# Performance work log

Measured on AMD Instinct MI355X. Metric: run time of the kernel, lower is better.

The kernel has to match this reference:

```python
import jax, jax.numpy as jnp
import numpy as np

B, T, D, NH, L = 8192, 100, 44, 64, 8  # batch, seq/ode steps, obs_dim, rnn hidden, latent


def setup_inputs() -> dict:
    key = jax.random.key(0)
    ks = jax.random.split(key, 12)
    s = 0.1
    return {
        "x": jax.random.normal(ks[0], (B, T, D), jnp.float32),
        "mask": jax.random.randint(ks[1], (B, T, D), 0, 2).astype(jnp.float32),
        "epsilon": jax.random.normal(ks[2], (B, L), jnp.float32),
        "Wi2h": jax.random.normal(ks[3], (D + NH, NH), jnp.float32) * s,
        "bi2h": jnp.zeros((NH,), jnp.float32),
        "Wh2o": jax.random.normal(ks[4], (NH, 2 * L), jnp.float32) * s,
        "bh2o": jnp.zeros((2 * L,), jnp.float32),
        "Wf1": jax.random.normal(ks[5], (L, NH), jnp.float32) * s,
        "bf1": jnp.zeros((NH,), jnp.float32),
        "Wf2": jax.random.normal(ks[6], (NH, NH), jnp.float32) * s,
        "bf2": jnp.zeros((NH,), jnp.float32),
        "Wf3": jax.random.normal(ks[7], (NH, L), jnp.float32) * s,
        "bf3": jnp.zeros((L,), jnp.float32),
        "Wd1": jax.random.normal(ks[8], (L, NH), jnp.float32) * s,
        "bd1": jnp.zeros((NH,), jnp.float32),
        "Wd2": jax.random.normal(ks[9], (NH, D), jnp.float32) * s,
        "bd2": jnp.zeros((D,), jnp.float32),
    }


def reference(x, mask, epsilon, Wi2h, bi2h, Wh2o, bh2o,
              Wf1, bf1, Wf2, bf2, Wf3, bf3, Wd1, bd1, Wd2, bd2):
    masked_x = x * mask  # [B,T,D]

    # --- reverse-time recognition RNN (scan over time, reversed) ---
    def rnn_step(h, obs):
        h = jnp.tanh(jnp.concatenate([obs, h], axis=1) @ Wi2h + bi2h)
        return h, None

    xs_rev = jnp.transpose(masked_x[:, ::-1, :], (1, 0, 2))  # [T,B,D]
    h0 = jnp.zeros((x.shape[0], Wi2h.shape[1]), x.dtype)
    h_final, _ = jax.lax.scan(rnn_step, h0, xs_rev)
    out = h_final @ Wh2o + bh2o  # [B,2L]
    qz0_mean, qz0_logvar = out[:, :L], out[:, L:]

    # reparameterized latent sample
    z0 = epsilon * jnp.exp(0.5 * qz0_logvar) + qz0_mean  # [B,L]

    # --- latent ODE dynamics, fixed-step RK4 over ts = linspace(0,1,100) ---
    def f(z):
        h1 = jax.nn.elu(z @ Wf1 + bf1)
        h2 = jax.nn.elu(h1 @ Wf2 + bf2)
        return h2 @ Wf3 + bf3

    dt = jnp.asarray(1.0 / (T - 1), x.dtype)

    def rk4_step(z, _):
        k1 = f(z)
        k2 = f(z + 0.5 * dt * k1)
        k3 = f(z + 0.5 * dt * k2)
        k4 = f(z + dt * k3)
        zn = z + (dt / 6.0) * (k1 + 2.0 * k2 + 2.0 * k3 + k4)
        return zn, zn

    _, zs = jax.lax.scan(rk4_step, z0, None, length=T - 1)  # [T-1,B,L]
    pred_z = jnp.transpose(jnp.concatenate([z0[None], zs], axis=0), (1, 0, 2))  # [B,T,L]

    # --- decoder ---
    pred_x = jax.nn.relu(pred_z @ Wd1 + bd1) @ Wd2 + bd2  # [B,T,D]

    # fill observed entries back in
    updated_x = jnp.where(masked_x != 0, masked_x, pred_x)

    # --- loss ---
    noise_logvar = 2.0 * jnp.log(jnp.asarray(0.3, x.dtype))
    log2pi = jnp.log(jnp.asarray(2.0 * np.pi, x.dtype))
    logpx = (-0.5 * (log2pi + noise_logvar +
                     (x - updated_x) ** 2 / jnp.exp(noise_logvar))).sum((-1, -2))  # [B]
    kl = (-0.5 * qz0_logvar + (jnp.exp(qz0_logvar) + qz0_mean ** 2) / 2.0 - 0.5).sum(-1)  # [B]
    loss = jnp.mean(-logpx + kl)
    return loss
```

## Files before the change

kernel.cpp:

```cpp
#include <hip/hip_runtime.h>
#include <stdint.h>


constexpr int B_ = 8192, T_ = 100, D_ = 44, NH_ = 64, L_ = 8;

typedef float f32x4 __attribute__((ext_vector_type(4)));
typedef uint32_t u32x2 __attribute__((ext_vector_type(2)));

#if __has_builtin(__builtin_amdgcn_mfma_f32_16x16x16bf16_1k)
typedef short frag16 __attribute__((ext_vector_type(4)));
#define MFMA16(a, b, c) __builtin_amdgcn_mfma_f32_16x16x16bf16_1k(a, b, c, 0, 0, 0)
#define USE_F16 0
#elif __has_builtin(__builtin_amdgcn_mfma_f32_16x16x16_bf16_1k)
typedef short frag16 __attribute__((ext_vector_type(4)));
#define MFMA16(a, b, c) __builtin_amdgcn_mfma_f32_16x16x16_bf16_1k(a, b, c, 0, 0, 0)
#define USE_F16 0
#elif __has_builtin(__builtin_amdgcn_mfma_f32_16x16x16_bf16)
typedef __bf16 frag16 __attribute__((ext_vector_type(4)));
#define MFMA16(a, b, c) __builtin_amdgcn_mfma_f32_16x16x16_bf16(a, b, c, 0, 0, 0)
#define USE_F16 0
#else
typedef _Float16 frag16 __attribute__((ext_vector_type(4)));
#define MFMA16(a, b, c) __builtin_amdgcn_mfma_f32_16x16x16f16(a, b, c, 0, 0, 0)
#define USE_F16 1
#endif

__device__ __forceinline__ float fexp2(float x) { return __builtin_amdgcn_exp2f(x); }
__device__ __forceinline__ float frcp(float x) { return __builtin_amdgcn_rcpf(x); }
__device__ __forceinline__ float fexp(float x) { return fexp2(x * 1.44269504088896341f); }
__device__ __forceinline__ float tanh_f(float x) {
  float e = fexp2(x * 2.88539008177792681f);
  return 1.0f - 2.0f * frcp(e + 1.0f);
}
__device__ __forceinline__ float elu_f(float x) { return x > 0.0f ? x : (fexp(x) - 1.0f); }

__device__ __forceinline__ uint32_t EW(float v) {
#if USE_F16
  return (uint32_t)__builtin_bit_cast(unsigned short, (_Float16)v);
#else
  return (uint32_t)__builtin_bit_cast(unsigned short, (__bf16)v);
#endif
}
__device__ __forceinline__ uint32_t PK2(float lo, float hi) { return EW(lo) | (EW(hi) << 16); }
__device__ __forceinline__ frag16 fr4(float a, float b, float c, float d) {
  u32x2 u = {PK2(a, b), PK2(c, d)};
  return __builtin_bit_cast(frag16, u);
}
__device__ __forceinline__ frag16 frpk(f32x4 v) {
  u32x2 u = {PK2(v[0], v[1]), PK2(v[2], v[3])};
  return __builtin_bit_cast(frag16, u);
}
__device__ __forceinline__ float f4get(const float4& f, int i) {
  return i == 0 ? f.x : (i == 1 ? f.y : (i == 2 ? f.z : f.w));
}

__global__ __launch_bounds__(128) void fused_kernel(
    const float* __restrict__ x, const float* __restrict__ mask,
    const float* __restrict__ eps,
    const float* __restrict__ Wi2h, const float* __restrict__ bi2h,
    const float* __restrict__ Wh2o, const float* __restrict__ bh2o,
    const float* __restrict__ Wf1, const float* __restrict__ bf1,
    const float* __restrict__ Wf2, const float* __restrict__ bf2,
    const float* __restrict__ Wf3, const float* __restrict__ bf3,
    const float* __restrict__ Wd1, const float* __restrict__ bd1,
    const float* __restrict__ Wd2, const float* __restrict__ bd2,
    float* __restrict__ part) {
  const int tid = threadIdx.x;
  const int wid = tid >> 6;
  const int lane = tid & 63;
  const int c = lane & 15, q = lane >> 4;
  const int r0 = blockIdx.x * 16;
  const f32x4 fzero = {0.f, 0.f, 0.f, 0.f};

  __shared__ __align__(16) uint32_t ring[6400];
  __shared__ __align__(16) float pcring[8192];
  __shared__ uint32_t flags[104];
  __shared__ uint32_t w1prog;
  __shared__ uint32_t w0cons;
  __shared__ float sse_sh;

  if (tid < 104) flags[tid] = 0u;
  if (tid == 0) { w1prog = 0u; w0cons = 0u; }
  __syncthreads();

  float klt = 0.0f;

  if (wid == 0) {
    frag16 Ah[4][4];
#pragma unroll
    for (int tau = 0; tau < 4; ++tau)
#pragma unroll
      for (int kc = 0; kc < 4; ++kc) {
        const int m = 16 * tau + c;
        float wv[4];
#pragma unroll
        for (int i = 0; i < 4; ++i) wv[i] = Wi2h[(44 + 16 * kc + 4 * q + i) * 64 + m];
        Ah[tau][kc] = fr4(wv[0], wv[1], wv[2], wv[3]);
      }
    frag16 Ah2o[4];
#pragma unroll
    for (int kc = 0; kc < 4; ++kc) {
      float wv[4];
#pragma unroll
      for (int i = 0; i < 4; ++i) wv[i] = Wh2o[(16 * kc + 4 * q + i) * 16 + c];
      Ah2o[kc] = fr4(wv[0], wv[1], wv[2], wv[3]);
    }
    f32x4 bo;
#pragma unroll
    for (int r = 0; r < 4; ++r) bo[r] = bh2o[4 * q + r];

    volatile uint32_t* vprod = &w1prog;
    volatile uint32_t* vcons = &w0cons;

    while (*vprod < 1u) __builtin_amdgcn_s_sleep(1);
    asm volatile("" ::: "memory");
    f32x4 pcur[4], pnext[4];
#pragma unroll
    for (int tau = 0; tau < 4; ++tau)
      pcur[tau] = *(const f32x4*)(pcring + tau * 256 + lane * 4);
    if (lane == 0) *vcons = 1u;

    f32x4 hc[4] = {};
#pragma unroll 1
    for (int s = 0; s < T_; ++s) {
      if ((s & 3) == 0) {
        const uint32_t need = (uint32_t)((s + 5 > T_) ? T_ : s + 5);
        while (*vprod < need) __builtin_amdgcn_s_sleep(1);
        asm volatile("" ::: "memory");
      }
      if (s < T_ - 1) {
        const int sl = (s + 1) & 7;
#pragma unroll
        for (int tau = 0; tau < 4; ++tau)
          pnext[tau] = *(const f32x4*)(pcring + sl * 1024 + tau * 256 + lane * 4);
        if (lane == 0) *vcons = (uint32_t)(s + 2);
      }

      frag16 bh[4];
#pragma unroll
      for (int tau = 0; tau < 4; ++tau) bh[tau] = frpk(hc[tau]);
#pragma unroll
      for (int tau = 0; tau < 4; ++tau) {
        f32x4 p0 = MFMA16(Ah[tau][0], bh[0], pcur[tau]);
        f32x4 p1 = MFMA16(Ah[tau][1], bh[1], fzero);
        f32x4 p2 = MFMA16(Ah[tau][2], bh[2], fzero);
        f32x4 p3 = MFMA16(Ah[tau][3], bh[3], fzero);
#pragma unroll
        for (int r = 0; r < 4; ++r)
          hc[tau][r] = tanh_f((p0[r] + p1[r]) + (p2[r] + p3[r]));
      }
#pragma unroll
      for (int tau = 0; tau < 4; ++tau) pcur[tau] = pnext[tau];
    }

    frag16 bhF[4];
#pragma unroll
    for (int tau = 0; tau < 4; ++tau) bhF[tau] = frpk(hc[tau]);
    f32x4 o = bo;
#pragma unroll
    for (int kc = 0; kc < 4; ++kc) o = MFMA16(Ah2o[kc], bhF[kc], o);

    float lv[4];
#pragma unroll
    for (int r = 0; r < 4; ++r)
      lv[r] = __int_as_float(__shfl(__float_as_int(o[r]), lane + 32, 64));

    f32x4 z = {};
    if (q < 2) {
      const float4 ev = *(const float4*)(eps + (size_t)(r0 + c) * 8 + 4 * q);
#pragma unroll
      for (int r = 0; r < 4; ++r) {
        const float m = o[r];
        z[r] = f4get(ev, r) * fexp(0.5f * lv[r]) + m;
        klt += -0.5f * lv[r] + (fexp(lv[r]) + m * m) * 0.5f - 0.5f;
      }
    }
    klt += __shfl_xor(klt, 1);  klt += __shfl_xor(klt, 2);
    klt += __shfl_xor(klt, 4);  klt += __shfl_xor(klt, 8);
    klt += __shfl_xor(klt, 16); klt += __shfl_xor(klt, 32);

    __builtin_amdgcn_sched_barrier(0);

    frag16 A1[4], A2[4][4], A3[4];
#pragma unroll
    for (int tau = 0; tau < 4; ++tau) {
      float w1[4];
#pragma unroll
      for (int i = 0; i < 4; ++i) {
        const int k = 4 * q + i;
        w1[i] = k < 8 ? Wf1[k * 64 + 16 * tau + c] : (k == 8 ? bf1[16 * tau + c] : 0.0f);
      }
      A1[tau] = fr4(w1[0], w1[1], w1[2], w1[3]);
    }
#pragma unroll
    for (int tau = 0; tau < 4; ++tau)
#pragma unroll
      for (int kc = 0; kc < 4; ++kc) {
        float wv[4];
#pragma unroll
        for (int i = 0; i < 4; ++i) wv[i] = Wf2[(16 * kc + 4 * q + i) * 64 + 16 * tau + c];
        A2[tau][kc] = fr4(wv[0], wv[1], wv[2], wv[3]);
      }
#pragma unroll
    for (int kc = 0; kc < 4; ++kc) {
      float wv[4];
#pragma unroll
      for (int i = 0; i < 4; ++i)
        wv[i] = (c < 8) ? Wf3[(16 * kc + 4 * q + i) * 8 + c] : 0.0f;
      A3[kc] = fr4(wv[0], wv[1], wv[2], wv[3]);
    }
    f32x4 b2_[4], b3_;
#pragma unroll
    for (int tau = 0; tau < 4; ++tau)
#pragma unroll
      for (int r = 0; r < 4; ++r) b2_[tau][r] = bf2[16 * tau + 4 * q + r];
#pragma unroll
    for (int r = 0; r < 4; ++r) b3_[r] = (q < 2) ? bf3[4 * q + r] : 0.0f;

    auto build_bz = [&](f32x4 zv) -> frag16 {
      u32x2 u = {PK2(zv[0], zv[1]), PK2(zv[2], zv[3])};
      if (q == 2) { u[0] = EW(1.0f); u[1] = 0u; }
      else if (q == 3) { u[0] = 0u; u[1] = 0u; }
      return __builtin_bit_cast(frag16, u);
    };

    auto feval = [&](frag16 bz) -> f32x4 {
      frag16 bh[4];
#pragma unroll
      for (int tau = 0; tau < 4; ++tau) {
        f32x4 h = MFMA16(A1[tau], bz, fzero);
#pragma unroll
        for (int r = 0; r < 4; ++r) h[r] = elu_f(h[r]);
        bh[tau] = frpk(h);
      }
      frag16 bg[4];
#pragma unroll
      for (int tau = 0; tau < 4; ++tau) {
        f32x4 g0 = MFMA16(A2[tau][0], bh[0], b2_[tau]);
        f32x4 g1 = MFMA16(A2[tau][1], bh[1], fzero);
        f32x4 g2 = MFMA16(A2[tau][2], bh[2], fzero);
        f32x4 g3 = MFMA16(A2[tau][3], bh[3], fzero);
        f32x4 g;
#pragma unroll
        for (int r = 0; r < 4; ++r) g[r] = elu_f((g0[r] + g1[r]) + (g2[r] + g3[r]));
        bg[tau] = frpk(g);
      }
      f32x4 r0_ = MFMA16(A3[0], bg[0], b3_);
      f32x4 r1_ = MFMA16(A3[1], bg[1], fzero);
      f32x4 r2_ = MFMA16(A3[2], bg[2], fzero);
      f32x4 r3_ = MFMA16(A3[3], bg[3], fzero);
      f32x4 rr;
#pragma unroll
      for (int r = 0; r < 4; ++r) rr[r] = (r0_[r] + r1_[r]) + (r2_[r] + r3_[r]);
      return rr;
    };

    const float dt = 1.0f / (float)(T_ - 1);
    const float hdt = 0.5f * dt;

#pragma unroll 1
    for (int t = 0; t < T_; ++t) {
      if (q < 2) {
        u32x2 v = {PK2(z[0], z[1]), PK2(z[2], z[3])};
        *(u32x2*)(ring + (t * 32 + c * 2 + q) * 2) = v;
      }
      asm volatile("" ::: "memory");
      if (lane == 0) ((volatile uint32_t*)flags)[t] = 1u;

      if (t < T_ - 1) {
        f32x4 k1 = feval(build_bz(z));
        f32x4 zt;
#pragma unroll
        for (int r = 0; r < 4; ++r) zt[r] = z[r] + hdt * k1[r];
        f32x4 k2 = feval(build_bz(zt));
#pragma unroll
        for (int r = 0; r < 4; ++r) zt[r] = z[r] + hdt * k2[r];
        f32x4 k3 = feval(build_bz(zt));
#pragma unroll
        for (int r = 0; r < 4; ++r) zt[r] = z[r] + dt * k3[r];
        f32x4 k4 = feval(build_bz(zt));
#pragma unroll
        for (int r = 0; r < 4; ++r)
          z[r] += (dt / 6.0f) * (k1[r] + 2.0f * (k2[r] + k3[r]) + k4[r]);
      }
    }
  } else {
    const frag16 fgbias = fr4(1.0f, 0.f, 0.f, 0.f);

    frag16 Ao[4][3];
#pragma unroll
    for (int tau = 0; tau < 4; ++tau)
#pragma unroll
      for (int kc = 0; kc < 3; ++kc) {
        const int m = 16 * tau + c;
        float wv[4];
#pragma unroll
        for (int i = 0; i < 4; ++i) {
          const int k = 64 + 16 * kc + 4 * q + i;
          float v = 0.0f;
          if (k < 108) v = Wi2h[(k - 64) * 64 + m];
          else if (k == 108) v = bi2h[m];
          wv[i] = v;
        }
        Ao[tau][kc] = fr4(wv[0], wv[1], wv[2], wv[3]);
      }

    const float* xrowbase = x + (size_t)(r0 + c) * T_ * D_;
    const float* mrowbase = mask + (size_t)(r0 + c) * T_ * D_;

    auto load_obs = [&](int t, float4* xv, float4* mv) {
      const float* xp = xrowbase + (size_t)t * D_;
      const float* mp = mrowbase + (size_t)t * D_;
      xv[0] = *(const float4*)(xp + 4 * q);
      mv[0] = *(const float4*)(mp + 4 * q);
      xv[1] = *(const float4*)(xp + 16 + 4 * q);
      mv[1] = *(const float4*)(mp + 16 + 4 * q);
      float4 zz = {0.f, 0.f, 0.f, 0.f};
      xv[2] = zz; mv[2] = zz;
      if (q < 3) {
        xv[2] = *(const float4*)(xp + 32 + 4 * q);
        mv[2] = *(const float4*)(mp + 32 + 4 * q);
      }
    };
    auto make_ob = [&](const float4* cx, const float4* cm, frag16* ob) {
#pragma unroll
      for (int j = 0; j < 2; ++j) {
        u32x2 u = {PK2(cx[j].x * cm[j].x, cx[j].y * cm[j].y),
                   PK2(cx[j].z * cm[j].z, cx[j].w * cm[j].w)};
        ob[j] = __builtin_bit_cast(frag16, u);
      }
      u32x2 u = {PK2(cx[2].x * cm[2].x, cx[2].y * cm[2].y),
                 PK2(cx[2].z * cm[2].z, cx[2].w * cm[2].w)};
      ob[2] = (q < 3) ? __builtin_bit_cast(frag16, u) : fgbias;
    };

    volatile uint32_t* vcons = &w0cons;
    volatile uint32_t* vprod = &w1prog;

    {
      float4 xo[3], mo[3];
      load_obs(T_ - 1, xo, mo);
#pragma unroll 1
      for (int s1 = 0; s1 < T_; ++s1) {
        const int t = T_ - 1 - s1;
        float4 cx[3], cm[3];
#pragma unroll
        for (int j = 0; j < 3; ++j) { cx[j] = xo[j]; cm[j] = mo[j]; }
        if (t > 0) load_obs(t - 1, xo, mo);

        frag16 ob[3];
        make_ob(cx, cm, ob);
        f32x4 pc[4];
#pragma unroll
        for (int tau = 0; tau < 4; ++tau)
          pc[tau] = MFMA16(Ao[tau][2], ob[2],
                           MFMA16(Ao[tau][1], ob[1],
                                  MFMA16(Ao[tau][0], ob[0], fzero)));

        while ((uint32_t)s1 >= *vcons + 8u) __builtin_amdgcn_s_sleep(1);
        asm volatile("" ::: "memory");
        const int sl = s1 & 7;
#pragma unroll
        for (int tau = 0; tau < 4; ++tau)
          *(f32x4*)(pcring + sl * 1024 + tau * 256 + lane * 4) = pc[tau];
        asm volatile("" ::: "memory");
        if (lane == 0) *vprod = (uint32_t)(s1 + 1);
      }
    }

    frag16 Ad1[4], Ad2[3][4];
#pragma unroll
    for (int tau = 0; tau < 4; ++tau) {
      float wd[4];
#pragma unroll
      for (int i = 0; i < 4; ++i) {
        const int k = 4 * q + i;
        wd[i] = k < 8 ? Wd1[k * 64 + 16 * tau + c] : (k == 8 ? bd1[16 * tau + c] : 0.0f);
      }
      Ad1[tau] = fr4(wd[0], wd[1], wd[2], wd[3]);
    }
#pragma unroll
    for (int tau = 0; tau < 3; ++tau)
#pragma unroll
      for (int kc = 0; kc < 4; ++kc) {
        const int m = 16 * tau + c;
        float wv[4];
#pragma unroll
        for (int i = 0; i < 4; ++i)
          wv[i] = (m < 44) ? Wd2[(16 * kc + 4 * q + i) * 44 + m] : 0.0f;
        Ad2[tau][kc] = fr4(wv[0], wv[1], wv[2], wv[3]);
      }
    f32x4 bd2_[3];
#pragma unroll
    for (int tau = 0; tau < 3; ++tau)
#pragma unroll
      for (int r = 0; r < 4; ++r) {
        const int d = 16 * tau + 4 * q + r;
        bd2_[tau][r] = (d < 44) ? bd2[d] : 0.0f;
      }

    float qacc = 0.0f;
    volatile uint32_t* vf = flags;

#pragma unroll 1
    for (int t = 0; t < T_; ++t) {
      float4 xc[3], mc[3];
#pragma unroll
      for (int tau = 0; tau < 3; ++tau) {
        const int d0 = 16 * tau + 4 * q;
        if (d0 < 44) {
          const size_t off = (size_t)(r0 + c) * T_ * D_ + (size_t)t * D_ + d0;
          xc[tau] = *(const float4*)(x + off);
          mc[tau] = *(const float4*)(mask + off);
        } else {
          float4 zz = {0.f, 0.f, 0.f, 0.f};
          xc[tau] = zz; mc[tau] = zz;
        }
      }

      while (vf[t] == 0u) __builtin_amdgcn_s_sleep(1);
      asm volatile("" ::: "memory");

      frag16 bz;
      {
        u32x2 u = {0u, 0u};
        if (q < 2) u = *(const u32x2*)(ring + (t * 32 + c * 2 + q) * 2);
        else if (q == 2) u[0] = EW(1.0f);
        bz = __builtin_bit_cast(frag16, u);
      }

      frag16 bhd[4];
#pragma unroll
      for (int tau = 0; tau < 4; ++tau) {
        f32x4 hd = MFMA16(Ad1[tau], bz, fzero);
#pragma unroll
        for (int r = 0; r < 4; ++r) hd[r] = fmaxf(hd[r], 0.0f);
        bhd[tau] = frpk(hd);
      }
#pragma unroll
      for (int tau = 0; tau < 3; ++tau) {
        f32x4 p0 = MFMA16(Ad2[tau][0], bhd[0], bd2_[tau]);
        f32x4 p1 = MFMA16(Ad2[tau][1], bhd[1], fzero);
        f32x4 p2 = MFMA16(Ad2[tau][2], bhd[2], fzero);
        f32x4 p3 = MFMA16(Ad2[tau][3], bhd[3], fzero);
        if (16 * tau + 4 * q < 44) {
#pragma unroll
          for (int r = 0; r < 4; ++r) {
            const float p = (p0[r] + p1[r]) + (p2[r] + p3[r]);
            const float xa = f4get(xc[tau], r), ma = f4get(mc[tau], r);
            const float mx = xa * ma;
            const float upd = (mx != 0.0f) ? mx : p;
            const float df = xa - upd;
            qacc += df * df;
          }
        }
      }
    }

    float tot = qacc * (0.5f / 0.09f);
    tot += __shfl_xor(tot, 1);  tot += __shfl_xor(tot, 2);
    tot += __shfl_xor(tot, 4);  tot += __shfl_xor(tot, 8);
    tot += __shfl_xor(tot, 16); tot += __shfl_xor(tot, 32);
    if (lane == 0) sse_sh = tot;
  }

  __syncthreads();
  if (tid == 0) part[blockIdx.x] = sse_sh + klt;
}

__global__ __launch_bounds__(512) void reduce_kernel(const float* __restrict__ part,
                                                     float* __restrict__ out) {
  __shared__ float s[8];
  const int tid = threadIdx.x;
  float v = part[tid];
  v += __shfl_xor(v, 1);  v += __shfl_xor(v, 2);
  v += __shfl_xor(v, 4);  v += __shfl_xor(v, 8);
  v += __shfl_xor(v, 16); v += __shfl_xor(v, 32);
  if ((tid & 63) == 0) s[tid >> 6] = v;
  __syncthreads();
  if (tid == 0) {
    float acc = 0.0f;
#pragma unroll
    for (int i = 0; i < 8; ++i) acc += s[i];
    const float c0 = 0.28503427112126353f;
    out[0] = acc * (1.0f / (float)B_) - (float)(T_ * D_) * c0;
  }
}

extern "C" void kernel_launch(void* const* d_in, const int* in_sizes, int n_in,
                              void* d_out, int out_size, void* d_ws, size_t ws_size,
                              hipStream_t stream) {
  const float* x    = (const float*)d_in[0];
  const float* mask = (const float*)d_in[1];
  const float* eps  = (const float*)d_in[2];
  const float* Wi2h = (const float*)d_in[3];
  const float* bi2h = (const float*)d_in[4];
  const float* Wh2o = (const float*)d_in[5];
  const float* bh2o = (const float*)d_in[6];
  const float* Wf1  = (const float*)d_in[7];
  const float* bf1  = (const float*)d_in[8];
  const float* Wf2  = (const float*)d_in[9];
  const float* bf2  = (const float*)d_in[10];
  const float* Wf3  = (const float*)d_in[11];
  const float* bf3  = (const float*)d_in[12];
  const float* Wd1  = (const float*)d_in[13];
  const float* bd1  = (const float*)d_in[14];
  const float* Wd2  = (const float*)d_in[15];
  const float* bd2  = (const float*)d_in[16];

  float* loss = (float*)d_out;
  float* part = (float*)d_ws;

  fused_kernel<<<dim3(B_ / 16), dim3(128), 0, stream>>>(
      x, mask, eps, Wi2h, bi2h, Wh2o, bh2o, Wf1, bf1, Wf2, bf2, Wf3, bf3,
      Wd1, bd1, Wd2, bd2, part);
  reduce_kernel<<<dim3(1), dim3(512), 0, stream>>>(part, loss);
}
```

Measured before the change: 681.2 us.

## Integrate RK4 in pre-activation space with fused Wf3·Wf1, offload z reconstruction to decoder wave

The ODE wave now carries u = z·Wf1 (the first-layer pre-activation) instead of z, using the precomputed product Wf3·Wf1 and bias bf3·Wf1. This removes the first-layer MFMA from every function evaluation and shortens the serial dependency chain per RK4 stage. The per-stage hidden activations are written to a double-buffered LDS slot. The decoder wave recomputes z by applying Wf3 to those activations and keeps a second copy of the RK4 update, with a new consumer counter for backpressure. The costs are rounding error from the fused bf16 weights and extra LDS traffic plus MFMA work on the second wave.

```diff
diff --git a/kernel.cpp b/kernel.cpp
--- a/kernel.cpp
+++ b/kernel.cpp
@@ -72,18 +72,21 @@
   const int r0 = blockIdx.x * 16;
   const f32x4 fzero = {0.f, 0.f, 0.f, 0.f};
 
-  __shared__ __align__(16) uint32_t ring[6400];
   __shared__ __align__(16) float pcring[8192];
+  __shared__ __align__(16) uint32_t bgbuf[4096];
+  __shared__ __align__(16) float zbuf[128];
   __shared__ uint32_t flags[104];
-  __shared__ uint32_t w1prog;
-  __shared__ uint32_t w0cons;
+  __shared__ uint32_t w1prog, w0cons;
+  __shared__ uint32_t w1cons, zflag;
   __shared__ float sse_sh;
 
   if (tid < 104) flags[tid] = 0u;
-  if (tid == 0) { w1prog = 0u; w0cons = 0u; }
+  if (tid == 0) { w1prog = 0u; w0cons = 0u; w1cons = 0u; zflag = 0u; }
   __syncthreads();
 
   float klt = 0.0f;
+  const float dt = 1.0f / (float)(T_ - 1);
+  const float hdt = 0.5f * dt;
 
   if (wid == 0) {
     frag16 Ah[4][4];
@@ -179,9 +182,13 @@
     klt += __shfl_xor(klt, 4);  klt += __shfl_xor(klt, 8);
     klt += __shfl_xor(klt, 16); klt += __shfl_xor(klt, 32);
 
+    if (q < 2) *(f32x4*)(zbuf + (c * 2 + q) * 4) = z;
+    asm volatile("" ::: "memory");
+    if (lane == 0) *((volatile uint32_t*)&zflag) = 1u;
+
     __builtin_amdgcn_sched_barrier(0);
 
-    frag16 A1[4], A2[4][4], A3[4];
+    frag16 A1[4], A2[4][4], W31f[4][4];
 #pragma unroll
     for (int tau = 0; tau < 4; ++tau) {
       float w1[4];
@@ -202,87 +209,121 @@
         A2[tau][kc] = fr4(wv[0], wv[1], wv[2], wv[3]);
       }
 #pragma unroll
-    for (int kc = 0; kc < 4; ++kc) {
-      float wv[4];
-#pragma unroll
-      for (int i = 0; i < 4; ++i)
-        wv[i] = (c < 8) ? Wf3[(16 * kc + 4 * q + i) * 8 + c] : 0.0f;
-      A3[kc] = fr4(wv[0], wv[1], wv[2], wv[3]);
-    }
-    f32x4 b2_[4], b3_;
+    for (int tau = 0; tau < 4; ++tau) {
+      const int m = 16 * tau + c;
+      float w1c[8];
+#pragma unroll
+      for (int l = 0; l < 8; ++l) w1c[l] = Wf1[l * 64 + m];
+#pragma unroll
+      for (int kc = 0; kc < 4; ++kc) {
+        float wv[4];
+#pragma unroll
+        for (int i = 0; i < 4; ++i) {
+          const int k = 16 * kc + 4 * q + i;
+          const float4 w3a = *(const float4*)(Wf3 + k * 8);
+          const float4 w3b = *(const float4*)(Wf3 + k * 8 + 4);
+          float acc = 0.0f;
+#pragma unroll
+          for (int l = 0; l < 4; ++l) acc += f4get(w3a, l) * w1c[l];
+#pragma unroll
+          for (int l = 0; l < 4; ++l) acc += f4get(w3b, l) * w1c[4 + l];
+          wv[i] = acc;
+        }
+        W31f[tau][kc] = fr4(wv[0], wv[1], wv[2], wv[3]);
+      }
+    }
+    f32x4 b2_[4], bwc[4];
 #pragma unroll
     for (int tau = 0; tau < 4; ++tau)
 #pragma unroll
-      for (int r = 0; r < 4; ++r) b2_[tau][r] = bf2[16 * tau + 4 * q + r];
-#pragma unroll
-    for (int r = 0; r < 4; ++r) b3_[r] = (q < 2) ? bf3[4 * q + r] : 0.0f;
-
-    auto build_bz = [&](f32x4 zv) -> frag16 {
-      u32x2 u = {PK2(zv[0], zv[1]), PK2(zv[2], zv[3])};
+      for (int r = 0; r < 4; ++r) {
+        b2_[tau][r] = bf2[16 * tau + 4 * q + r];
+        const int m = 16 * tau + 4 * q + r;
+        float acc = 0.0f;
+#pragma unroll
+        for (int l = 0; l < 8; ++l) acc += bf3[l] * Wf1[l * 64 + m];
+        bwc[tau][r] = acc;
+      }
+
+    frag16 bz0;
+    {
+      u32x2 u = {PK2(z[0], z[1]), PK2(z[2], z[3])};
       if (q == 2) { u[0] = EW(1.0f); u[1] = 0u; }
       else if (q == 3) { u[0] = 0u; u[1] = 0u; }
-      return __builtin_bit_cast(frag16, u);
-    };
-
-    auto feval = [&](frag16 bz) -> f32x4 {
-      frag16 bh[4];
+      bz0 = __builtin_bit_cast(frag16, u);
+    }
+    f32x4 uS[4];
+#pragma unroll
+    for (int tau = 0; tau < 4; ++tau) uS[tau] = MFMA16(A1[tau], bz0, fzero);
+
+    auto feval_u = [&](const f32x4* uc, uint32_t* bgslot, f32x4* ku) {
+      frag16 bh2[4];
 #pragma unroll
       for (int tau = 0; tau < 4; ++tau) {
-        f32x4 h = MFMA16(A1[tau], bz, fzero);
-#pragma unroll
-        for (int r = 0; r < 4; ++r) h[r] = elu_f(h[r]);
-        bh[tau] = frpk(h);
+        f32x4 h;
+#pragma unroll
+        for (int r = 0; r < 4; ++r) h[r] = elu_f(uc[tau][r]);
+        bh2[tau] = frpk(h);
       }
       frag16 bg[4];
 #pragma unroll
       for (int tau = 0; tau < 4; ++tau) {
-        f32x4 g0 = MFMA16(A2[tau][0], bh[0], b2_[tau]);
-        f32x4 g1 = MFMA16(A2[tau][1], bh[1], fzero);
-        f32x4 g2 = MFMA16(A2[tau][2], bh[2], fzero);
-        f32x4 g3 = MFMA16(A2[tau][3], bh[3], fzero);
+        f32x4 g0 = MFMA16(A2[tau][0], bh2[0], b2_[tau]);
+        f32x4 g1 = MFMA16(A2[tau][1], bh2[1], fzero);
+        f32x4 g2 = MFMA16(A2[tau][2], bh2[2], fzero);
+        f32x4 g3 = MFMA16(A2[tau][3], bh2[3], fzero);
         f32x4 g;
 #pragma unroll
         for (int r = 0; r < 4; ++r) g[r] = elu_f((g0[r] + g1[r]) + (g2[r] + g3[r]));
         bg[tau] = frpk(g);
-      }
-      f32x4 r0_ = MFMA16(A3[0], bg[0], b3_);
-      f32x4 r1_ = MFMA16(A3[1], bg[1], fzero);
-      f32x4 r2_ = MFMA16(A3[2], bg[2], fzero);
-      f32x4 r3_ = MFMA16(A3[3], bg[3], fzero);
-      f32x4 rr;
-#pragma unroll
-      for (int r = 0; r < 4; ++r) rr[r] = (r0_[r] + r1_[r]) + (r2_[r] + r3_[r]);
-      return rr;
+        *(u32x2*)(bgslot + tau * 128 + lane * 2) =
+            __builtin_bit_cast(u32x2, bg[tau]);
+      }
+#pragma unroll
+      for (int tau = 0; tau < 4; ++tau) {
+        f32x4 k0 = MFMA16(W31f[tau][0], bg[0], bwc[tau]);
+        f32x4 k1_ = MFMA16(W31f[tau][1], bg[1], fzero);
+        f32x4 k2_ = MFMA16(W31f[tau][2], bg[2], fzero);
+        f32x4 k3_ = MFMA16(W31f[tau][3], bg[3], fzero);
+#pragma unroll
+        for (int r = 0; r < 4; ++r)
+          ku[tau][r] = (k0[r] + k1_[r]) + (k2_[r] + k3_[r]);
+      }
     };
 
-    const float dt = 1.0f / (float)(T_ - 1);
-    const float hdt = 0.5f * dt;
-
+    volatile uint32_t* vw1c = &w1cons;
 #pragma unroll 1
-    for (int t = 0; t < T_; ++t) {
-      if (q < 2) {
-        u32x2 v = {PK2(z[0], z[1]), PK2(z[2], z[3])};
-        *(u32x2*)(ring + (t * 32 + c * 2 + q) * 2) = v;
-      }
+    for (int t = 0; t < T_ - 1; ++t) {
+      while ((int)*vw1c < t - 1) __builtin_amdgcn_s_sleep(1);
+      asm volatile("" ::: "memory");
+      uint32_t* bgp = bgbuf + (size_t)(t & 1) * 2048;
+
+      f32x4 ku1[4], ku2[4], ku3[4], ku4[4], ut[4];
+      feval_u(uS, bgp + 0 * 512, ku1);
+#pragma unroll
+      for (int tau = 0; tau < 4; ++tau)
+#pragma unroll
+        for (int r = 0; r < 4; ++r) ut[tau][r] = uS[tau][r] + hdt * ku1[tau][r];
+      feval_u(ut, bgp + 1 * 512, ku2);
+#pragma unroll
+      for (int tau = 0; tau < 4; ++tau)
+#pragma unroll
+        for (int r = 0; r < 4; ++r) ut[tau][r] = uS[tau][r] + hdt * ku2[tau][r];
+      feval_u(ut, bgp + 2 * 512, ku3);
+#pragma unroll
+      for (int tau = 0; tau < 4; ++tau)
+#pragma unroll
+        for (int r = 0; r < 4; ++r) ut[tau][r] = uS[tau][r] + dt * ku3[tau][r];
+      feval_u(ut, bgp + 3 * 512, ku4);
+#pragma unroll
+      for (int tau = 0; tau < 4; ++tau)
+#pragma unroll
+        for (int r = 0; r < 4; ++r)
+          uS[tau][r] += (dt / 6.0f) *
+              (ku1[tau][r] + 2.0f * (ku2[tau][r] + ku3[tau][r]) + ku4[tau][r]);
+
       asm volatile("" ::: "memory");
       if (lane == 0) ((volatile uint32_t*)flags)[t] = 1u;
-
-      if (t < T_ - 1) {
-        f32x4 k1 = feval(build_bz(z));
-        f32x4 zt;
-#pragma unroll
-        for (int r = 0; r < 4; ++r) zt[r] = z[r] + hdt * k1[r];
-        f32x4 k2 = feval(build_bz(zt));
-#pragma unroll
-        for (int r = 0; r < 4; ++r) zt[r] = z[r] + hdt * k2[r];
-        f32x4 k3 = feval(build_bz(zt));
-#pragma unroll
-        for (int r = 0; r < 4; ++r) zt[r] = z[r] + dt * k3[r];
-        f32x4 k4 = feval(build_bz(zt));
-#pragma unroll
-        for (int r = 0; r < 4; ++r)
-          z[r] += (dt / 6.0f) * (k1[r] + 2.0f * (k2[r] + k3[r]) + k4[r]);
-      }
     }
   } else {
     const frag16 fgbias = fr4(1.0f, 0.f, 0.f, 0.f);
@@ -336,6 +377,7 @@
 
     volatile uint32_t* vcons = &w0cons;
     volatile uint32_t* vprod = &w1prog;
+    const f32x4 fz0 = {0.f, 0.f, 0.f, 0.f};
 
     {
       float4 xo[3], mo[3];
@@ -355,7 +397,7 @@
         for (int tau = 0; tau < 4; ++tau)
           pc[tau] = MFMA16(Ao[tau][2], ob[2],
                            MFMA16(Ao[tau][1], ob[1],
-                                  MFMA16(Ao[tau][0], ob[0], fzero)));
+                                  MFMA16(Ao[tau][0], ob[0], fz0)));
 
         while ((uint32_t)s1 >= *vcons + 8u) __builtin_amdgcn_s_sleep(1);
         asm volatile("" ::: "memory");
@@ -368,7 +410,7 @@
       }
     }
 
-    frag16 Ad1[4], Ad2[3][4];
+    frag16 Ad1[4], Ad2[3][4], A3[4];
 #pragma unroll
     for (int tau = 0; tau < 4; ++tau) {
       float wd[4];
@@ -390,7 +432,15 @@
           wv[i] = (m < 44) ? Wd2[(16 * kc + 4 * q + i) * 44 + m] : 0.0f;
         Ad2[tau][kc] = fr4(wv[0], wv[1], wv[2], wv[3]);
       }
-    f32x4 bd2_[3];
+#pragma unroll
+    for (int kc = 0; kc < 4; ++kc) {
+      float wv[4];
+#pragma unroll
+      for (int i = 0; i < 4; ++i)
+        wv[i] = (c < 8) ? Wf3[(16 * kc + 4 * q + i) * 8 + c] : 0.0f;
+      A3[kc] = fr4(wv[0], wv[1], wv[2], wv[3]);
+    }
+    f32x4 bd2_[3], b3_;
 #pragma unroll
     for (int tau = 0; tau < 3; ++tau)
 #pragma unroll
@@ -398,9 +448,17 @@
         const int d = 16 * tau + 4 * q + r;
         bd2_[tau][r] = (d < 44) ? bd2[d] : 0.0f;
       }
+#pragma unroll
+    for (int r = 0; r < 4; ++r) b3_[r] = (q < 2) ? bf3[4 * q + r] : 0.0f;
+
+    while (*((volatile uint32_t*)&zflag) == 0u) __builtin_amdgcn_s_sleep(1);
+    asm volatile("" ::: "memory");
+    f32x4 z = {};
+    if (q < 2) z = *(const f32x4*)(zbuf + (c * 2 + q) * 4);
 
     float qacc = 0.0f;
     volatile uint32_t* vf = flags;
+    volatile uint32_t* vw1c = &w1cons;
 
 #pragma unroll 1
     for (int t = 0; t < T_; ++t) {
@@ -418,21 +476,17 @@
         }
       }
 
-      while (vf[t] == 0u) __builtin_amdgcn_s_sleep(1);
-      asm volatile("" ::: "memory");
-
       frag16 bz;
       {
-        u32x2 u = {0u, 0u};
-        if (q < 2) u = *(const u32x2*)(ring + (t * 32 + c * 2 + q) * 2);
-        else if (q == 2) u[0] = EW(1.0f);
+        u32x2 u = {PK2(z[0], z[1]), PK2(z[2], z[3])};
+        if (q == 2) { u[0] = EW(1.0f); u[1] = 0u; }
+        else if (q == 3) { u[0] = 0u; u[1] = 0u; }
         bz = __builtin_bit_cast(frag16, u);
       }
-
       frag16 bhd[4];
 #pragma unroll
       for (int tau = 0; tau < 4; ++tau) {
-        f32x4 hd = MFMA16(Ad1[tau], bz, fzero);
+        f32x4 hd = MFMA16(Ad1[tau], bz, fz0);
 #pragma unroll
         for (int r = 0; r < 4; ++r) hd[r] = fmaxf(hd[r], 0.0f);
         bhd[tau] = frpk(hd);
@@ -440,9 +494,9 @@
 #pragma unroll
       for (int tau = 0; tau < 3; ++tau) {
         f32x4 p0 = MFMA16(Ad2[tau][0], bhd[0], bd2_[tau]);
-        f32x4 p1 = MFMA16(Ad2[tau][1], bhd[1], fzero);
-        f32x4 p2 = MFMA16(Ad2[tau][2], bhd[2], fzero);
-        f32x4 p3 = MFMA16(Ad2[tau][3], bhd[3], fzero);
+        f32x4 p1 = MFMA16(Ad2[tau][1], bhd[1], fz0);
+        f32x4 p2 = MFMA16(Ad2[tau][2], bhd[2], fz0);
+        f32x4 p3 = MFMA16(Ad2[tau][3], bhd[3], fz0);
         if (16 * tau + 4 * q < 44) {
 #pragma unroll
           for (int r = 0; r < 4; ++r) {
@@ -454,6 +508,32 @@
             qacc += df * df;
           }
         }
+      }
+
+      if (t < T_ - 1) {
+        while (vf[t] == 0u) __builtin_amdgcn_s_sleep(1);
+        asm volatile("" ::: "memory");
+        const uint32_t* bgp = bgbuf + (size_t)(t & 1) * 2048;
+        f32x4 kk[4];
+#pragma unroll
+        for (int fe = 0; fe < 4; ++fe) {
+          frag16 bg[4];
+#pragma unroll
+          for (int tau = 0; tau < 4; ++tau)
+            bg[tau] = __builtin_bit_cast(frag16,
+                *(const u32x2*)(bgp + fe * 512 + tau * 128 + lane * 2));
+          f32x4 r0_ = MFMA16(A3[0], bg[0], b3_);
+          f32x4 r1_ = MFMA16(A3[1], bg[1], fz0);
+          f32x4 r2_ = MFMA16(A3[2], bg[2], fz0);
+          f32x4 r3_ = MFMA16(A3[3], bg[3], fz0);
+#pragma unroll
+          for (int r = 0; r < 4; ++r) kk[fe][r] = (r0_[r] + r1_[r]) + (r2_[r] + r3_[r]);
+        }
+#pragma unroll
+        for (int r = 0; r < 4; ++r)
+          z[r] += (dt / 6.0f) * (kk[0][r] + 2.0f * (kk[1][r] + kk[2][r]) + kk[3][r]);
+        asm volatile("" ::: "memory");
+        if (lane == 0) *vw1c = (uint32_t)(t + 1);
       }
     }
 
```

Result: slower. 748.6 us (+9.9%).
